# Optimization experiments

Measured on AMD Instinct MI355X. Metric: run time of the kernel, lower is better.

The kernel has to match this reference:

```python
import jax, jax.numpy as jnp
import numpy as np

B, T, I, H = 64, 512, 512, 512


def setup_inputs() -> dict:
    key = jax.random.key(0)
    ks = jax.random.split(key, 7)
    xavier_std = float(np.sqrt(2.0 / (B + H)))  # matches xavier_normal_ on [B,H]
    w_scale = float(1.0 / np.sqrt(H))           # ~ pytorch LSTMCell default scale
    return {
        "x": jax.random.normal(ks[0], (B, T, I), dtype=jnp.float32),
        "h0": jax.random.normal(ks[1], (B, H), dtype=jnp.float32) * xavier_std,
        "c0": jax.random.normal(ks[2], (B, H), dtype=jnp.float32) * xavier_std,
        "W_ih": jax.random.normal(ks[3], (4 * H, I), dtype=jnp.float32) * w_scale,
        "W_hh": jax.random.normal(ks[4], (4 * H, H), dtype=jnp.float32) * w_scale,
        "b_ih": jax.random.normal(ks[5], (4 * H,), dtype=jnp.float32) * w_scale,
        "b_hh": jax.random.normal(ks[6], (4 * H,), dtype=jnp.float32) * w_scale,
    }


def lstm_forward(x, h0, c0, W_ih, W_hh, b_ih, b_hh):
    # Precompute the input-to-gate projection for all timesteps in one big GEMM.
    # xg: [T, B, 4H]
    xg = jnp.einsum("bti,gi->tbg", x, W_ih) + (b_ih + b_hh)

    def step(carry, xg_t):
        h, c = carry
        gates = xg_t + h @ W_hh.T  # [B, 4H]
        i, f, g, o = jnp.split(gates, 4, axis=-1)
        i = jax.nn.sigmoid(i)
        f = jax.nn.sigmoid(f)
        g = jnp.tanh(g)
        o = jax.nn.sigmoid(o)
        c = f * c + i * g
        h = o * jnp.tanh(c)
        return (h, c), h

    (h_T, c_T), outs = jax.lax.scan(step, (h0, c0), xg)
    output = jnp.transpose(outs, (1, 0, 2))  # [B, T, H]
    return output, h_T, c_T


def reference(x, h0, c0, W_ih, W_hh, b_ih, b_hh):
    return lstm_forward(x, h0, c0, W_ih, W_hh, b_ih, b_hh)
```

## Files before the change

### kernel.cpp

```cpp
#include <hip/hip_runtime.h>
#include <hip/hip_fp16.h>
#include <string.h>

constexpr int B = 64, T = 512, I = 512, H = 512, G = 2048;

typedef _Float16 half8 __attribute__((ext_vector_type(8)));
typedef float floatx4 __attribute__((ext_vector_type(4)));

__global__ __launch_bounds__(256, 2) void xg_gemm(
    const float* __restrict__ x,
    const float* __restrict__ W_ih,
    const float* __restrict__ b_ih,
    const float* __restrict__ b_hh,
    _Float16* __restrict__ xg)
{
    const int tid  = threadIdx.x;
    const int wave = tid >> 6, lane = tid & 63;
    const int quad = lane >> 4, col = lane & 15;
    const int rowA = blockIdx.x * 128 + wave * 16;
    const int rowB = rowA + 64;

    __shared__ __align__(16) _Float16 xs[64][264];

    half8 wfA[16], wfB[16];
    {
        const float* wpA = W_ih + (size_t)(rowA + col) * I;
        const float* wpB = W_ih + (size_t)(rowB + col) * I;
#pragma unroll
        for (int kc = 0; kc < 16; ++kc) {
            half8 vA, vB;
#pragma unroll
            for (int j = 0; j < 8; ++j) {
                vA[j] = (_Float16)wpA[kc * 32 + quad * 8 + j];
                vB[j] = (_Float16)wpB[kc * 32 + quad * 8 + j];
            }
            wfA[kc] = vA; wfB[kc] = vB;
        }
    }
    float biasA[4], biasB[4];
#pragma unroll
    for (int r = 0; r < 4; ++r) {
        biasA[r] = b_ih[rowA + quad * 4 + r] + b_hh[rowA + quad * 4 + r];
        biasB[r] = b_ih[rowB + quad * 4 + r] + b_hh[rowB + quad * 4 + r];
    }

    for (int ti = 0; ti < 4; ++ti) {
        const int t = blockIdx.y * 4 + ti;
        floatx4 accA[4], accB[4];
#pragma unroll
        for (int nt = 0; nt < 4; ++nt) {
            accA[nt] = (floatx4){0.f, 0.f, 0.f, 0.f};
            accB[nt] = (floatx4){0.f, 0.f, 0.f, 0.f};
        }

        for (int hfl = 0; hfl < 2; ++hfl) {
            __syncthreads();
#pragma unroll 4
            for (int c = 0; c < 16; ++c) {
                int idx = c * 256 + tid;
                int row = idx >> 6;
                int kk  = (idx & 63) * 4;
                const float4 v = *(const float4*)(x + ((size_t)row * T + t) * I + hfl * 256 + kk);
                xs[row][kk + 0] = (_Float16)v.x;
                xs[row][kk + 1] = (_Float16)v.y;
                xs[row][kk + 2] = (_Float16)v.z;
                xs[row][kk + 3] = (_Float16)v.w;
            }
            __syncthreads();
#pragma unroll
            for (int kc = 0; kc < 8; ++kc) {
#pragma unroll
                for (int nt = 0; nt < 4; ++nt) {
                    const half8 bfr = *(const half8*)&xs[nt * 16 + col][kc * 32 + quad * 8];
                    accA[nt] = __builtin_amdgcn_mfma_f32_16x16x32_f16(
                        wfA[hfl * 8 + kc], bfr, accA[nt], 0, 0, 0);
                    accB[nt] = __builtin_amdgcn_mfma_f32_16x16x32_f16(
                        wfB[hfl * 8 + kc], bfr, accB[nt], 0, 0, 0);
                }
            }
        }
#pragma unroll
        for (int nt = 0; nt < 4; ++nt) {
            int b = nt * 16 + col;
#pragma unroll
            for (int r = 0; r < 4; ++r) {
                xg[((size_t)t * G + rowA + quad * 4 + r) * B + b] = (_Float16)(accA[nt][r] + biasA[r]);
                xg[((size_t)t * G + rowB + quad * 4 + r) * B + b] = (_Float16)(accB[nt][r] + biasB[r]);
            }
        }
    }
}

__global__ __launch_bounds__(256, 1) void lstm_rec(
    const float* __restrict__ h0,
    const float* __restrict__ c0,
    const float* __restrict__ W_hh,
    const _Float16* __restrict__ xg,
    _Float16* __restrict__ hbuf,
    unsigned int* __restrict__ cnts,
    float* __restrict__ out)
{
    const int blk  = blockIdx.x;
    const int bg   = blk & 3;
    const int hg   = blk >> 2;
    const int tid  = threadIdx.x;
    const int wave = tid >> 6, lane = tid & 63;
    const int quad = lane >> 4, col = lane & 15;

    const int bglob = bg * 16 + col;
    const int hbase = hg * 32 + wave * 8;

    unsigned int* cnt = cnts + bg * 64;

    int arow0 = (col < 8) ? (hbase + col) : (512 + hbase + col - 8);
    int arow1 = arow0 + 1024;
    half8 wf0[16], wf1[16];
#pragma unroll
    for (int kc = 0; kc < 16; ++kc) {
        const float* p0 = W_hh + (size_t)arow0 * H + kc * 32 + quad * 8;
        const float* p1 = W_hh + (size_t)arow1 * H + kc * 32 + quad * 8;
        half8 v0, v1;
#pragma unroll
        for (int j = 0; j < 8; ++j) { v0[j] = (_Float16)p0[j]; v1[j] = (_Float16)p1[j]; }
        wf0[kc] = v0; wf1[kc] = v1;
    }

    int xrow0[4], xrow1[4];
#pragma unroll
    for (int r = 0; r < 4; ++r) {
        int lr = quad * 4 + r;
        xrow0[r] = (lr < 8) ? (hbase + lr) : (512 + hbase + lr - 8);
        xrow1[r] = xrow0[r] + 1024;
    }

    float c[4];
#pragma unroll
    for (int r = 0; r < 4; ++r)
        c[r] = c0[(size_t)bglob * H + hbase + (quad & 1) * 4 + r];

    _Float16* hb0 = hbuf + ((size_t)0 * 4 + bg) * 16 * 512;
    _Float16* hb1 = hbuf + ((size_t)1 * 4 + bg) * 16 * 512;

    if (quad < 2) {
        _Float16 v4[4];
#pragma unroll
        for (int r = 0; r < 4; ++r)
            v4[r] = (_Float16)h0[(size_t)bglob * H + hbase + (quad & 1) * 4 + r];
        unsigned long long uv; __builtin_memcpy(&uv, v4, 8);
        __hip_atomic_store((unsigned long long*)(hb0 + (size_t)col * 512 + hbase + (quad & 1) * 4),
                           uv, __ATOMIC_RELAXED, __HIP_MEMORY_SCOPE_AGENT);
    }
    asm volatile("s_waitcnt vmcnt(0)" ::: "memory");
    __syncthreads();
    if (tid == 0)
        __hip_atomic_fetch_add(cnt, 1u, __ATOMIC_RELAXED, __HIP_MEMORY_SCOPE_AGENT);

    float xp0[4], xp1[4];
#pragma unroll
    for (int r = 0; r < 4; ++r) {
        xp0[r] = (float)xg[(size_t)xrow0[r] * B + bglob];
        xp1[r] = (float)xg[(size_t)xrow1[r] * B + bglob];
    }

    while (__hip_atomic_load(cnt, __ATOMIC_RELAXED, __HIP_MEMORY_SCOPE_AGENT) < 16u) {}
    asm volatile("" ::: "memory");

    float hh[4] = {0.f, 0.f, 0.f, 0.f};

    for (int t = 0; t < T; ++t) {
        const _Float16* hcur = (t & 1) ? hb1 : hb0;
        _Float16*       hnxt = (t & 1) ? hb0 : hb1;

        unsigned long long hu0[16], hu1[16];
#pragma unroll
        for (int kc = 0; kc < 16; ++kc) {
            unsigned long long* hp =
                (unsigned long long*)(hcur + (size_t)col * 512 + kc * 32 + quad * 8);
            hu0[kc] = __hip_atomic_load(hp,     __ATOMIC_RELAXED, __HIP_MEMORY_SCOPE_AGENT);
            hu1[kc] = __hip_atomic_load(hp + 1, __ATOMIC_RELAXED, __HIP_MEMORY_SCOPE_AGENT);
        }

        floatx4 acc0 = (floatx4){0.f, 0.f, 0.f, 0.f};
        floatx4 acc1 = (floatx4){0.f, 0.f, 0.f, 0.f};
#pragma unroll
        for (int kc = 0; kc < 16; ++kc) {
            half8 bfr;
            __builtin_memcpy(&bfr, &hu0[kc], 8);
            __builtin_memcpy((char*)&bfr + 8, &hu1[kc], 8);
            acc0 = __builtin_amdgcn_mfma_f32_16x16x32_f16(wf0[kc], bfr, acc0, 0, 0, 0);
            acc1 = __builtin_amdgcn_mfma_f32_16x16x32_f16(wf1[kc], bfr, acc1, 0, 0, 0);
        }

        float p0[4], p1[4];
#pragma unroll
        for (int r = 0; r < 4; ++r) {
            p0[r] = acc0[r] + xp0[r];
            p1[r] = acc1[r] + xp1[r];
        }
        float e0[4], e1[4];
#pragma unroll
        for (int r = 0; r < 4; ++r) {
            e0[r] = __shfl_xor(p0[r], 32);
            e1[r] = __shfl_xor(p1[r], 32);
        }
#pragma unroll
        for (int r = 0; r < 4; ++r) {
            float iv = (quad < 2) ? p0[r] : e0[r];
            float fv = (quad < 2) ? e0[r] : p0[r];
            float gv = (quad < 2) ? p1[r] : e1[r];
            float ov = (quad < 2) ? e1[r] : p1[r];
            float ii = 1.f / (1.f + __expf(-iv));
            float ff = 1.f / (1.f + __expf(-fv));
            float eg = __expf(-2.f * gv);
            float gg = (1.f - eg) / (1.f + eg);
            float oo = 1.f / (1.f + __expf(-ov));
            float cn = ff * c[r] + ii * gg;
            c[r] = cn;
            float ec = __expf(-2.f * cn);
            hh[r] = oo * ((1.f - ec) / (1.f + ec));
        }
        if (quad < 2) {
            _Float16 v4[4] = {(_Float16)hh[0], (_Float16)hh[1],
                              (_Float16)hh[2], (_Float16)hh[3]};
            unsigned long long uv; __builtin_memcpy(&uv, v4, 8);
            __hip_atomic_store((unsigned long long*)(hnxt + (size_t)col * 512 + hbase + (quad & 1) * 4),
                               uv, __ATOMIC_RELAXED, __HIP_MEMORY_SCOPE_AGENT);
            float* op = out + ((size_t)bglob * T + t) * H + hbase + (quad & 1) * 4;
            op[0] = hh[0]; op[1] = hh[1]; op[2] = hh[2]; op[3] = hh[3];
        }

        asm volatile("s_waitcnt vmcnt(0)" ::: "memory");
        __syncthreads();
        if (tid == 0)
            __hip_atomic_fetch_add(cnt, 1u, __ATOMIC_RELAXED, __HIP_MEMORY_SCOPE_AGENT);

        if (t + 1 < T) {
            const _Float16* xgt = xg + (size_t)(t + 1) * G * B;
#pragma unroll
            for (int r = 0; r < 4; ++r) {
                xp0[r] = (float)xgt[(size_t)xrow0[r] * B + bglob];
                xp1[r] = (float)xgt[(size_t)xrow1[r] * B + bglob];
            }
            const unsigned int tgt = 16u * (unsigned)(t + 2);
            while (__hip_atomic_load(cnt, __ATOMIC_RELAXED, __HIP_MEMORY_SCOPE_AGENT) < tgt) {}
            asm volatile("" ::: "memory");
        }
    }

    if (quad < 2) {
        float* hT = out + (size_t)B * T * H;
        float* cT = hT + (size_t)B * H;
#pragma unroll
        for (int r = 0; r < 4; ++r) {
            int jj = (quad & 1) * 4 + r;
            hT[(size_t)bglob * H + hbase + jj] = hh[r];
            cT[(size_t)bglob * H + hbase + jj] = c[r];
        }
    }
}

extern "C" void kernel_launch(void* const* d_in, const int* in_sizes, int n_in,
                              void* d_out, int out_size, void* d_ws, size_t ws_size,
                              hipStream_t stream) {
    const float* x    = (const float*)d_in[0];
    const float* h0   = (const float*)d_in[1];
    const float* c0   = (const float*)d_in[2];
    const float* W_ih = (const float*)d_in[3];
    const float* W_hh = (const float*)d_in[4];
    const float* b_ih = (const float*)d_in[5];
    const float* b_hh = (const float*)d_in[6];
    float* out = (float*)d_out;

    unsigned int* cnts = (unsigned int*)d_ws;
    _Float16* hbuf = (_Float16*)((char*)d_ws + 2048);
    _Float16* xg   = (_Float16*)((char*)d_ws + 2048 + (size_t)2 * 4 * 16 * 512 * 2);

    hipMemsetAsync(d_ws, 0, 2048, stream);

    xg_gemm<<<dim3(16, 128), 256, 0, stream>>>(x, W_ih, b_ih, b_hh, xg);
    lstm_rec<<<64, 256, 0, stream>>>(h0, c0, W_hh, xg, hbuf, cnts, out);
}
```

Measured before the change: 3.126 ms.

## Replace atomic counter barrier with per-block flags polled by one wave

Swaps the shared fetch_add counter per batch group for 16 per-block flag words. Each block stores its step number to its own flag, and only wave 0 polls all 16 flags with 64-bit loads before a __syncthreads. The output store is moved after the flag publish and vectorised to float4, so it no longer sits on the critical path before the barrier signal. This is meant to remove atomic contention and cut polling traffic from every thread, at the cost of an extra block-level barrier per step.

```diff
diff --git a/kernel.cpp b/kernel.cpp
--- a/kernel.cpp
+++ b/kernel.cpp
@@ -97,7 +97,7 @@
     const float* __restrict__ W_hh,
     const _Float16* __restrict__ xg,
     _Float16* __restrict__ hbuf,
-    unsigned int* __restrict__ cnts,
+    unsigned int* __restrict__ flags,
     float* __restrict__ out)
 {
     const int blk  = blockIdx.x;
@@ -110,7 +110,8 @@
     const int bglob = bg * 16 + col;
     const int hbase = hg * 32 + wave * 8;
 
-    unsigned int* cnt = cnts + bg * 64;
+    unsigned int* myflag = flags + bg * 16 + hg;
+    const unsigned long long* fq = (const unsigned long long*)(flags + bg * 16);
 
     int arow0 = (col < 8) ? (hbase + col) : (512 + hbase + col - 8);
     int arow1 = arow0 + 1024;
@@ -153,7 +154,7 @@
     asm volatile("s_waitcnt vmcnt(0)" ::: "memory");
     __syncthreads();
     if (tid == 0)
-        __hip_atomic_fetch_add(cnt, 1u, __ATOMIC_RELAXED, __HIP_MEMORY_SCOPE_AGENT);
+        __hip_atomic_store(myflag, 1u, __ATOMIC_RELAXED, __HIP_MEMORY_SCOPE_AGENT);
 
     float xp0[4], xp1[4];
 #pragma unroll
@@ -162,8 +163,15 @@
         xp1[r] = (float)xg[(size_t)xrow1[r] * B + bglob];
     }
 
-    while (__hip_atomic_load(cnt, __ATOMIC_RELAXED, __HIP_MEMORY_SCOPE_AGENT) < 16u) {}
-    asm volatile("" ::: "memory");
+    if (wave == 0) {
+        for (;;) {
+            unsigned long long v = __hip_atomic_load(fq + (lane & 7),
+                                                     __ATOMIC_RELAXED, __HIP_MEMORY_SCOPE_AGENT);
+            unsigned mn = min((unsigned)v, (unsigned)(v >> 32));
+            if (__all(mn >= 1u)) break;
+        }
+    }
+    __syncthreads();
 
     float hh[4] = {0.f, 0.f, 0.f, 0.f};
 
@@ -219,21 +227,25 @@
             float ec = __expf(-2.f * cn);
             hh[r] = oo * ((1.f - ec) / (1.f + ec));
         }
+
         if (quad < 2) {
             _Float16 v4[4] = {(_Float16)hh[0], (_Float16)hh[1],
                               (_Float16)hh[2], (_Float16)hh[3]};
             unsigned long long uv; __builtin_memcpy(&uv, v4, 8);
             __hip_atomic_store((unsigned long long*)(hnxt + (size_t)col * 512 + hbase + (quad & 1) * 4),
                                uv, __ATOMIC_RELAXED, __HIP_MEMORY_SCOPE_AGENT);
-            float* op = out + ((size_t)bglob * T + t) * H + hbase + (quad & 1) * 4;
-            op[0] = hh[0]; op[1] = hh[1]; op[2] = hh[2]; op[3] = hh[3];
         }
 
         asm volatile("s_waitcnt vmcnt(0)" ::: "memory");
         __syncthreads();
         if (tid == 0)
-            __hip_atomic_fetch_add(cnt, 1u, __ATOMIC_RELAXED, __HIP_MEMORY_SCOPE_AGENT);
-
+            __hip_atomic_store(myflag, (unsigned)(t + 2),
+                               __ATOMIC_RELAXED, __HIP_MEMORY_SCOPE_AGENT);
+
+        if (quad < 2) {
+            float* op = out + ((size_t)bglob * T + t) * H + hbase + (quad & 1) * 4;
+            *(float4*)op = (float4){hh[0], hh[1], hh[2], hh[3]};
+        }
         if (t + 1 < T) {
             const _Float16* xgt = xg + (size_t)(t + 1) * G * B;
 #pragma unroll
@@ -241,9 +253,16 @@
                 xp0[r] = (float)xgt[(size_t)xrow0[r] * B + bglob];
                 xp1[r] = (float)xgt[(size_t)xrow1[r] * B + bglob];
             }
-            const unsigned int tgt = 16u * (unsigned)(t + 2);
-            while (__hip_atomic_load(cnt, __ATOMIC_RELAXED, __HIP_MEMORY_SCOPE_AGENT) < tgt) {}
-            asm volatile("" ::: "memory");
+            const unsigned tgt = (unsigned)(t + 2);
+            if (wave == 0) {
+                for (;;) {
+                    unsigned long long v = __hip_atomic_load(fq + (lane & 7),
+                                                             __ATOMIC_RELAXED, __HIP_MEMORY_SCOPE_AGENT);
+                    unsigned mn = min((unsigned)v, (unsigned)(v >> 32));
+                    if (__all(mn >= tgt)) break;
+                }
+            }
+            __syncthreads();
         }
     }
 
@@ -271,12 +290,12 @@
     const float* b_hh = (const float*)d_in[6];
     float* out = (float*)d_out;
 
-    unsigned int* cnts = (unsigned int*)d_ws;
+    unsigned int* flags = (unsigned int*)d_ws;
     _Float16* hbuf = (_Float16*)((char*)d_ws + 2048);
     _Float16* xg   = (_Float16*)((char*)d_ws + 2048 + (size_t)2 * 4 * 16 * 512 * 2);
 
     hipMemsetAsync(d_ws, 0, 2048, stream);
 
     xg_gemm<<<dim3(16, 128), 256, 0, stream>>>(x, W_ih, b_ih, b_hh, xg);
-    lstm_rec<<<64, 256, 0, stream>>>(h0, c0, W_hh, xg, hbuf, cnts, out);
+    lstm_rec<<<64, 256, 0, stream>>>(h0, c0, W_hh, xg, hbuf, flags, out);
 }
```

Result: slower. 3.238 ms (+3.6%).
